# Optimization experiments

Measured on AMD Instinct MI355X. Metric: run time of the kernel, lower is better.

The kernel has to match this reference:

```python
import jax, jax.numpy as jnp
import numpy as np

N_COMPANY = 16384
N_SECTOR = 64
PER_SECTOR = N_COMPANY // N_SECTOR  # 256, companies grouped contiguously by sector
WIN = 32
D_IN = 16
H_GRU = 64
H_INTRA = 64
H_INTER = 64
D_OUT = 4
E_INNER = 524288  # avg degree 32 within sectors


def setup_inputs() -> dict:
    key = jax.random.key(0)
    ks = jax.random.split(key, 20)
    s = 0.05

    daily_data_batch = jax.random.normal(ks[0], (WIN, N_COMPANY, D_IN), jnp.float32)

    rng = np.random.default_rng(0)
    dst = rng.integers(0, N_COMPANY, E_INNER)
    src = (dst // PER_SECTOR) * PER_SECTOR + rng.integers(0, PER_SECTOR, E_INNER)  # same-sector neighbors
    inner_edge = jnp.asarray(np.stack([src, dst]), jnp.int32)

    a, b = np.meshgrid(np.arange(N_SECTOR), np.arange(N_SECTOR), indexing="ij")
    oe = np.stack([a.ravel(), b.ravel()])
    oe = oe[:, oe[0] != oe[1]]  # fully-connected sector graph w/o self loops (GAT adds them)
    outer_edge = jnp.asarray(oe, jnp.int32)

    sector_ids = jnp.asarray(np.arange(N_COMPANY) // PER_SECTOR, jnp.int32)

    inp = {
        "daily_data_batch": daily_data_batch,
        "inner_edge": inner_edge,
        "outer_edge": outer_edge,
        "sector_ids": sector_ids,
        # BatchNorm1d(input_dim*window_size)
        "bn_gamma": jnp.ones((D_IN * WIN,), jnp.float32),
        "bn_beta": jnp.zeros((D_IN * WIN,), jnp.float32),
        # Graph GRU (per-node learnable initial hidden state)
        "gru_Wih": s * jax.random.normal(ks[1], (D_IN, 3 * H_GRU), jnp.float32),
        "gru_Whh": s * jax.random.normal(ks[2], (H_GRU, 3 * H_GRU), jnp.float32),
        "gru_bih": jnp.zeros((3 * H_GRU,), jnp.float32),
        "gru_bhh": jnp.zeros((3 * H_GRU,), jnp.float32),
        "gru_h0": s * jax.random.normal(ks[3], (N_COMPANY, H_GRU), jnp.float32),
        # intra-sector GATConv
        "gat1_W": s * jax.random.normal(ks[4], (H_GRU, H_INTRA), jnp.float32),
        "gat1_asrc": s * jax.random.normal(ks[5], (H_INTRA,), jnp.float32),
        "gat1_adst": s * jax.random.normal(ks[6], (H_INTRA,), jnp.float32),
        "gat1_b": jnp.zeros((H_INTRA,), jnp.float32),
        # inter-sector GATConv
        "gat2_W": s * jax.random.normal(ks[7], (H_INTRA, H_INTER), jnp.float32),
        "gat2_asrc": s * jax.random.normal(ks[8], (H_INTER,), jnp.float32),
        "gat2_adst": s * jax.random.normal(ks[9], (H_INTER,), jnp.float32),
        "gat2_b": jnp.zeros((H_INTER,), jnp.float32),
        # fusion / logit heads
        "fusion_W": s * jax.random.normal(ks[10], (H_GRU + H_INTRA + H_INTER, H_GRU), jnp.float32),
        "fusion_b": jnp.zeros((H_GRU,), jnp.float32),
        "logit_W": s * jax.random.normal(ks[11], (H_GRU, D_OUT), jnp.float32),
        "logit_b": jnp.zeros((D_OUT,), jnp.float32),
    }
    return inp


def _gat(x, edge, W, a_src, a_dst, b):
    """PyG-style single-head GATConv with default add_self_loops=True."""
    N = x.shape[0]
    h = x @ W  # [N, F]
    loops = jnp.arange(N, dtype=edge.dtype)
    src = jnp.concatenate([edge[0], loops])
    dst = jnp.concatenate([edge[1], loops])
    e = jax.nn.leaky_relu(h[src] @ a_src + h[dst] @ a_dst, 0.2)  # [E]
    # segment softmax over incoming edges per dst node
    m = jax.ops.segment_max(e, dst, num_segments=N)
    ex = jnp.exp(e - m[dst])
    denom = jax.ops.segment_sum(ex, dst, num_segments=N)
    alpha = ex / (denom[dst] + 1e-16)
    out = jax.ops.segment_sum(h[src] * alpha[:, None], dst, num_segments=N)
    return out + b


def _forward(daily_data_batch, inner_edge, outer_edge, sector_ids,
             bn_gamma, bn_beta,
             gru_Wih, gru_Whh, gru_bih, gru_bhh, gru_h0,
             gat1_W, gat1_asrc, gat1_adst, gat1_b,
             gat2_W, gat2_asrc, gat2_adst, gat2_b,
             fusion_W, fusion_b, logit_W, logit_b):
    W, N, D = daily_data_batch.shape
    # BatchNorm1d over companies (train-mode batch stats, eps=1e-5)
    xb = jnp.transpose(daily_data_batch, (1, 0, 2)).reshape(N, W * D)
    mu = xb.mean(axis=0)
    var = xb.var(axis=0)
    xb = (xb - mu) * jax.lax.rsqrt(var + 1e-5) * bn_gamma + bn_beta
    x = jnp.transpose(xb.reshape(N, W, D), (1, 0, 2))  # [W, N, D]

    # GRU over the window, per-node hidden state
    def step(h, xt):
        gi = xt @ gru_Wih + gru_bih
        gh = h @ gru_Whh + gru_bhh
        ir, iz, inn = jnp.split(gi, 3, axis=-1)
        hr, hz, hn = jnp.split(gh, 3, axis=-1)
        r = jax.nn.sigmoid(ir + hr)
        z = jax.nn.sigmoid(iz + hz)
        n = jnp.tanh(inn + r * hn)
        return (1.0 - z) * n + z * h, None

    seq_emb, _ = jax.lax.scan(step, gru_h0, x)  # [N, H_GRU]

    intra_emb = _gat(seq_emb, inner_edge, gat1_W, gat1_asrc, gat1_adst, gat1_b)  # [N, H_INTRA]

    # sector_separater + per-sector max pooling == segment_max
    sec_pool = jax.ops.segment_max(intra_emb, sector_ids, num_segments=N_SECTOR)  # [S, H_INTRA]
    sec_emb = _gat(sec_pool, outer_edge, gat2_W, gat2_asrc, gat2_adst, gat2_b)  # [S, H_INTER]
    sec_broad = sec_emb[sector_ids]  # repeat_interleave back to companies

    fusion_vec = jnp.concatenate([seq_emb, sec_broad, intra_emb], axis=-1)
    fusion_vec = jax.nn.relu(fusion_vec @ fusion_W + fusion_b)
    logits = jax.nn.softmax(fusion_vec @ logit_W + logit_b, axis=1)
    logits = jnp.cumsum(logits, axis=1)
    eps = 5e-08
    return jnp.clip(logits, eps, 1.0 - eps)


def reference(daily_data_batch, inner_edge, outer_edge, sector_ids,
              bn_gamma, bn_beta,
              gru_Wih, gru_Whh, gru_bih, gru_bhh, gru_h0,
              gat1_W, gat1_asrc, gat1_adst, gat1_b,
              gat2_W, gat2_asrc, gat2_adst, gat2_b,
              fusion_W, fusion_b, logit_W, logit_b):
    return _forward(daily_data_batch, inner_edge, outer_edge, sector_ids,
                    bn_gamma, bn_beta,
                    gru_Wih, gru_Whh, gru_bih, gru_bhh, gru_h0,
                    gat1_W, gat1_asrc, gat1_adst, gat1_b,
                    gat2_W, gat2_asrc, gat2_adst, gat2_b,
                    fusion_W, fusion_b, logit_W, logit_b)
```

## Files before the change

kernel.cpp:

```cpp
#include <hip/hip_runtime.h>

#define NC 16384
#define WIN 32
#define DI 16
#define EI 524288

typedef unsigned short u16;
typedef unsigned char u8;
typedef unsigned int u32;
typedef __attribute__((ext_vector_type(8))) short bfrag8;
typedef __attribute__((ext_vector_type(4))) float facc4;

__device__ __forceinline__ float bf2f(u16 u) { return __uint_as_float(((u32)u) << 16); }
__device__ __forceinline__ u16 f2bf(float f) {
    u32 u = __float_as_uint(f);
    u += 0x7FFFu + ((u >> 16) & 1u);
    return (u16)(u >> 16);
}
__device__ __forceinline__ float frcp(float x) { return __builtin_amdgcn_rcpf(x); }
__device__ __forceinline__ float lrelu(float x) { return x >= 0.0f ? x : 0.2f * x; }
__device__ __forceinline__ float loadf(const void* p, size_t i, bool f32) {
    return f32 ? ((const float*)p)[i] : bf2f(((const u16*)p)[i]);
}
__device__ __forceinline__ bool is_f32(const void* gamma) {
    return ((const u32*)gamma)[0] == 0x3F800000u;
}

#define O_SCALE 0
#define O_SHIFT 512
#define O_WIH   1024
#define O_WHH   4096
#define O_BIH   16384
#define O_BHH   16576
#define O_G1W   16768
#define O_G1AS  20864
#define O_G1AD  20928
#define O_G1B   20992
#define O_G2W   21056
#define O_G2AS  25152
#define O_G2AD  25216
#define O_G2B   25280
#define O_FB    25344
#define O_LW    25408
#define O_LB    25664
#define O_FW16  25668
#define O_BNACC 31812
#define O_SEQ   40960
#define O_H1    1089536
#define O_INTRA 1613824
#define O_SPOOL 2138112
#define O_AS    2158592
#define O_AD    2174976
#define O_M     2191360

__global__ __launch_bounds__(256) void k_convert(const void* __restrict__ gamma,
                                                 const void* __restrict__ wih,
                                                 const void* __restrict__ whh,
                                                 const void* __restrict__ bih,
                                                 const void* __restrict__ bhh,
                                                 const void* __restrict__ g1w,
                                                 const void* __restrict__ g1as,
                                                 const void* __restrict__ g1ad,
                                                 const void* __restrict__ g1b,
                                                 const void* __restrict__ g2w,
                                                 const void* __restrict__ g2as,
                                                 const void* __restrict__ g2ad,
                                                 const void* __restrict__ g2b,
                                                 const void* __restrict__ fw,
                                                 const void* __restrict__ fb,
                                                 const void* __restrict__ lw,
                                                 const void* __restrict__ lb,
                                                 float* __restrict__ ws) {
    int gt = blockIdx.x * 256 + threadIdx.x;
    const int GS = 64 * 256;
    bool f32 = is_f32(gamma);
    u16* fw16 = (u16*)(ws + O_FW16);
    for (int i = gt; i < 3072; i += GS) ws[O_WIH + i] = loadf(wih, i, f32);
    for (int i = gt; i < 12288; i += GS) {
        ws[O_WHH + i] = loadf(whh, i, f32);
        fw16[i] = f32 ? f2bf(((const float*)fw)[i]) : ((const u16*)fw)[i];
    }
    for (int i = gt; i < 192; i += GS) {
        ws[O_BIH + i] = loadf(bih, i, f32);
        ws[O_BHH + i] = loadf(bhh, i, f32);
    }
    for (int i = gt; i < 4096; i += GS) {
        ws[O_G1W + i] = loadf(g1w, i, f32);
        ws[O_G2W + i] = loadf(g2w, i, f32);
    }
    if (gt < 64) {
        ws[O_G1AS + gt] = loadf(g1as, gt, f32);
        ws[O_G1AD + gt] = loadf(g1ad, gt, f32);
        ws[O_G1B + gt] = loadf(g1b, gt, f32);
        ws[O_G2AS + gt] = loadf(g2as, gt, f32);
        ws[O_G2AD + gt] = loadf(g2ad, gt, f32);
        ws[O_G2B + gt] = loadf(g2b, gt, f32);
        ws[O_FB + gt] = loadf(fb, gt, f32);
    }
    if (gt < 256) ws[O_LW + gt] = loadf(lw, gt, f32);
    if (gt < 4) ws[O_LB + gt] = loadf(lb, gt, f32);
    for (int i = gt; i < 1024; i += GS) ws[O_BNACC + i] = 0.f;
}

__global__ __launch_bounds__(256) void k_bnpart(const void* __restrict__ daily,
                                                const void* __restrict__ gamma,
                                                float* __restrict__ bnacc) {
    __shared__ float rS[256 * 17];
    __shared__ float rQ[256 * 17];
    int w = blockIdx.x >> 2, ch = blockIdx.x & 3;
    int tid = threadIdx.x;
    bool f32 = is_f32(gamma);
    float s[16], q[16];
#pragma unroll
    for (int i = 0; i < 16; i++) { s[i] = 0.f; q[i] = 0.f; }
    for (int it = 0; it < 16; it++) {
        int c = ch * 4096 + it * 256 + tid;
        size_t base = ((size_t)w * NC + c) * DI;
        float v[16];
        if (f32) {
            const float4* p = (const float4*)((const float*)daily + base);
            float4 a = p[0], b = p[1], cc = p[2], d = p[3];
            v[0] = a.x; v[1] = a.y; v[2] = a.z; v[3] = a.w;
            v[4] = b.x; v[5] = b.y; v[6] = b.z; v[7] = b.w;
            v[8] = cc.x; v[9] = cc.y; v[10] = cc.z; v[11] = cc.w;
            v[12] = d.x; v[13] = d.y; v[14] = d.z; v[15] = d.w;
        } else {
            const uint4* p = (const uint4*)((const u16*)daily + base);
            uint4 a = p[0], b = p[1];
            u32 us[8] = {a.x, a.y, a.z, a.w, b.x, b.y, b.z, b.w};
#pragma unroll
            for (int i = 0; i < 8; i++) {
                v[2 * i] = __uint_as_float(us[i] << 16);
                v[2 * i + 1] = __uint_as_float(us[i] & 0xFFFF0000u);
            }
        }
#pragma unroll
        for (int i = 0; i < 16; i++) { s[i] += v[i]; q[i] += v[i] * v[i]; }
    }
#pragma unroll
    for (int i = 0; i < 16; i++) { rS[tid * 17 + i] = s[i]; rQ[tid * 17 + i] = q[i]; }
    __syncthreads();
    int f = tid & 15, g = tid >> 4;
    float ss = 0.f, qq = 0.f;
    for (int t = g * 16; t < g * 16 + 16; t++) { ss += rS[t * 17 + f]; qq += rQ[t * 17 + f]; }
    atomicAdd(&bnacc[w * 16 + f], ss);
    atomicAdd(&bnacc[512 + w * 16 + f], qq);
}

__global__ __launch_bounds__(256) void k_edge(const int* __restrict__ edges, u32* __restrict__ M32) {
    int g = blockIdx.x * 256 + threadIdx.x;
    int4 s4 = ((const int4*)edges)[g];
    int4 d4 = ((const int4*)(edges + EI))[g];
    int ss[4] = {s4.x, s4.y, s4.z, s4.w};
    int dd[4] = {d4.x, d4.y, d4.z, d4.w};
#pragma unroll
    for (int i = 0; i < 4; i++) {
        int sl = ss[i] & 255;
        atomicAdd(&M32[dd[i] * 64 + (sl >> 2)], 1u << ((sl & 3) * 8));
    }
}

__global__ __launch_bounds__(256, 4) void k_gru(const void* __restrict__ daily,
                                                const void* __restrict__ gamma,
                                                const void* __restrict__ beta,
                                                const void* __restrict__ h0_g,
                                                const float* __restrict__ ws,
                                                float* __restrict__ seq_out,
                                                u16* __restrict__ h1_out,
                                                float* __restrict__ asg,
                                                float* __restrict__ adg) {
    __shared__ __attribute__((aligned(16))) u16 sHd[2][16 * 72];
    __shared__ __attribute__((aligned(16))) u16 sXall[512 * 24];
    __shared__ float sSc[512], sSh[512];
    __shared__ float sRed[2][4][16];
    int tid = threadIdx.x;
    int w = tid >> 6, lane = tid & 63;
    int li = lane & 15, q = lane >> 4;
    int col = w * 16 + li;
    int n0 = blockIdx.x * 16;
    bool f32 = is_f32(gamma);

    for (int f = tid; f < 512; f += 256) {
        float mu = ws[O_BNACC + f] * (1.0f / NC);
        float var = ws[O_BNACC + 512 + f] * (1.0f / NC) - mu * mu;
        float sc = loadf(gamma, f, f32) * rsqrtf(var + 1e-5f);
        sSc[f] = sc;
        sSh[f] = loadf(beta, f, f32) - mu * sc;
    }
    __syncthreads();
    for (int R = tid; R < 512; R += 256) {
        int t = R >> 4, m = R & 15;
        size_t base = ((size_t)t * NC + n0 + m) * DI;
        float xv[16];
        if (f32) {
            const float4* p = (const float4*)((const float*)daily + base);
            float4 a = p[0], b = p[1], c = p[2], d = p[3];
            xv[0] = a.x; xv[1] = a.y; xv[2] = a.z; xv[3] = a.w;
            xv[4] = b.x; xv[5] = b.y; xv[6] = b.z; xv[7] = b.w;
            xv[8] = c.x; xv[9] = c.y; xv[10] = c.z; xv[11] = c.w;
            xv[12] = d.x; xv[13] = d.y; xv[14] = d.z; xv[15] = d.w;
        } else {
            const uint4* p = (const uint4*)((const u16*)daily + base);
            uint4 a = p[0], b = p[1];
            u32 us[8] = {a.x, a.y, a.z, a.w, b.x, b.y, b.z, b.w};
#pragma unroll
            for (int i = 0; i < 8; i++) {
                xv[2 * i] = __uint_as_float(us[i] << 16);
                xv[2 * i + 1] = __uint_as_float(us[i] & 0xFFFF0000u);
            }
        }
        u16 px[16];
#pragma unroll
        for (int i = 0; i < 16; i++) px[i] = f2bf(xv[i] * sSc[t * 16 + i] + sSh[t * 16 + i]);
        *(uint4*)&sXall[R * 24] = *(const uint4*)&px[0];
        *(uint4*)&sXall[R * 24 + 8] = *(const uint4*)&px[8];
    }

    bfrag8 bh[3][2], bx[3];
#pragma unroll
    for (int g = 0; g < 3; g++) {
        float sc = (g < 2) ? -1.0f : -2.0f;
#pragma unroll
        for (int kc = 0; kc < 2; kc++)
#pragma unroll
            for (int j = 0; j < 8; j++) {
                int k = kc * 32 + q * 8 + j;
                bh[g][kc][j] = (short)f2bf(sc * ws[O_WHH + k * 192 + g * 64 + col]);
            }
#pragma unroll
        for (int j = 0; j < 8; j++) {
            int k = q * 8 + j;
            bx[g][j] = (k < 16) ? (short)f2bf(sc * ws[O_WIH + k * 192 + g * 64 + col]) : (short)0;
        }
    }
    float bR = -1.0f * (ws[O_BIH + col] + ws[O_BHH + col]);
    float bZ = -1.0f * (ws[O_BIH + 64 + col] + ws[O_BHH + 64 + col]);
    float bNX = -2.0f * ws[O_BIH + 128 + col];
    float bNH = -2.0f * ws[O_BHH + 128 + col];

    float hC[4];
#pragma unroll
    for (int r = 0; r < 4; r++)
        hC[r] = loadf(h0_g, (size_t)(n0 + q * 4 + r) * 64 + col, f32);
    if (tid < 128) {
        int hr = tid >> 3, hc = (tid & 7) * 8;
        u16 hrow[8];
#pragma unroll
        for (int i = 0; i < 8; i++)
            hrow[i] = f2bf(loadf(h0_g, (size_t)(n0 + hr) * 64 + hc + i, f32));
        *(uint4*)&sHd[0][hr * 72 + hc] = *(const uint4*)&hrow[0];
    }
    __syncthreads();

    bool xl = (q < 2);
    for (int t = 0; t < WIN; t++) {
        int p = t & 1;
        bfrag8 ax = (bfrag8){0, 0, 0, 0, 0, 0, 0, 0};
        if (xl) ax = *(const bfrag8*)&sXall[(t * 16 + li) * 24 + q * 8];
        bfrag8 ah0 = *(const bfrag8*)&sHd[p][li * 72 + q * 8];
        bfrag8 ah1 = *(const bfrag8*)&sHd[p][li * 72 + 32 + q * 8];
        facc4 aR = __builtin_amdgcn_mfma_f32_16x16x32_bf16(ah0, bh[0][0], (facc4){bR, bR, bR, bR}, 0, 0, 0);
        facc4 aZ = __builtin_amdgcn_mfma_f32_16x16x32_bf16(ah0, bh[1][0], (facc4){bZ, bZ, bZ, bZ}, 0, 0, 0);
        facc4 aNH = __builtin_amdgcn_mfma_f32_16x16x32_bf16(ah0, bh[2][0], (facc4){bNH, bNH, bNH, bNH}, 0, 0, 0);
        facc4 aNX = __builtin_amdgcn_mfma_f32_16x16x32_bf16(ax, bx[2], (facc4){bNX, bNX, bNX, bNX}, 0, 0, 0);
        aR = __builtin_amdgcn_mfma_f32_16x16x32_bf16(ah1, bh[0][1], aR, 0, 0, 0);
        aZ = __builtin_amdgcn_mfma_f32_16x16x32_bf16(ah1, bh[1][1], aZ, 0, 0, 0);
        aNH = __builtin_amdgcn_mfma_f32_16x16x32_bf16(ah1, bh[2][1], aNH, 0, 0, 0);
        aR = __builtin_amdgcn_mfma_f32_16x16x32_bf16(ax, bx[0], aR, 0, 0, 0);
        aZ = __builtin_amdgcn_mfma_f32_16x16x32_bf16(ax, bx[1], aZ, 0, 0, 0);
#pragma unroll
        for (int r = 0; r < 4; r++) {
            float gr = frcp(1.0f + __expf(aR[r]));
            float gz = frcp(1.0f + __expf(aZ[r]));
            float narg = aNX[r] + gr * aNH[r];
            float gn = 2.0f * frcp(1.0f + __expf(narg)) - 1.0f;
            hC[r] = gn + gz * (hC[r] - gn);
        }
#pragma unroll
        for (int r = 0; r < 4; r++)
            sHd[p ^ 1][(q * 4 + r) * 72 + col] = f2bf(hC[r]);
        __syncthreads();
    }

#pragma unroll
    for (int r = 0; r < 4; r++)
        seq_out[(size_t)(n0 + q * 4 + r) * 64 + col] = hC[r];

    const facc4 zf = {0.f, 0.f, 0.f, 0.f};
    bfrag8 a0 = *(const bfrag8*)&sHd[0][li * 72 + q * 8];
    bfrag8 a1 = *(const bfrag8*)&sHd[0][li * 72 + 32 + q * 8];
    bfrag8 bg0, bg1;
#pragma unroll
    for (int j = 0; j < 8; j++) {
        bg0[j] = (short)f2bf(ws[O_G1W + (q * 8 + j) * 64 + col]);
        bg1[j] = (short)f2bf(ws[O_G1W + (32 + q * 8 + j) * 64 + col]);
    }
    facc4 acc = __builtin_amdgcn_mfma_f32_16x16x32_bf16(a0, bg0, zf, 0, 0, 0);
    acc = __builtin_amdgcn_mfma_f32_16x16x32_bf16(a1, bg1, acc, 0, 0, 0);
    float a1s_j = ws[O_G1AS + col], a1d_j = ws[O_G1AD + col];
    float pAs[4], pAd[4];
#pragma unroll
    for (int r = 0; r < 4; r++) {
        h1_out[(size_t)(n0 + q * 4 + r) * 64 + col] = f2bf(acc[r]);
        pAs[r] = acc[r] * a1s_j;
        pAd[r] = acc[r] * a1d_j;
    }
#pragma unroll
    for (int o = 1; o < 16; o <<= 1) {
#pragma unroll
        for (int r = 0; r < 4; r++) {
            pAs[r] += __shfl_xor(pAs[r], o);
            pAd[r] += __shfl_xor(pAd[r], o);
        }
    }
    if (li == 0) {
#pragma unroll
        for (int r = 0; r < 4; r++) {
            sRed[0][w][q * 4 + r] = pAs[r];
            sRed[1][w][q * 4 + r] = pAd[r];
        }
    }
    __syncthreads();
    if (tid < 16) {
        asg[n0 + tid] = sRed[0][0][tid] + sRed[0][1][tid] + sRed[0][2][tid] + sRed[0][3][tid];
        adg[n0 + tid] = sRed[1][0][tid] + sRed[1][1][tid] + sRed[1][2][tid] + sRed[1][3][tid];
    }
}

__global__ __launch_bounds__(256) void k_gat1agg(const u16* __restrict__ h1g,
                                                 const float* __restrict__ ws,
                                                 const u8* __restrict__ M8,
                                                 const float* __restrict__ asg,
                                                 const float* __restrict__ adg,
                                                 u16* __restrict__ intra,
                                                 float* __restrict__ spool4) {
    __shared__ __attribute__((aligned(16))) u16 hT[64 * 264];
    __shared__ __attribute__((aligned(16))) u16 sP[64 * 136];
    __shared__ float sAs[256], sAd[64], sB[64], sRS[64];
    __shared__ float sRSp[4][64];
    __shared__ float wmax[4];
    int tid = threadIdx.x;
    int sector = blockIdx.x >> 2;
    int dstbase = sector * 256 + (blockIdx.x & 3) * 64;
    int sbase = sector * 256;
    {
        const u16* row = h1g + (size_t)(sbase + tid) * 64;
#pragma unroll
        for (int c = 0; c < 16; c++) {
            uint2 v = ((const uint2*)row)[c];
            hT[(c * 4 + 0) * 264 + tid] = (u16)(v.x & 0xffff);
            hT[(c * 4 + 1) * 264 + tid] = (u16)(v.x >> 16);
            hT[(c * 4 + 2) * 264 + tid] = (u16)(v.y & 0xffff);
            hT[(c * 4 + 3) * 264 + tid] = (u16)(v.y >> 16);
        }
    }
    sAs[tid] = asg[sbase + tid];
    if (tid < 64) { sAd[tid] = adg[dstbase + tid]; sB[tid] = ws[O_G1B + tid]; }
    __syncthreads();
    int lane = tid & 63, w = tid >> 6;
    int li = lane & 15, q = lane >> 4;
    {
        float a = sAs[tid];
#pragma unroll
        for (int o = 1; o < 64; o <<= 1) a = fmaxf(a, __shfl_xor(a, o));
        if (lane == 0) wmax[w] = a;
    }
    __syncthreads();
    float maxA = fmaxf(fmaxf(wmax[0], wmax[1]), fmaxf(wmax[2], wmax[3]));

    int prow = tid >> 2, pcg = tid & 3;
    float adr_p = sAd[prow];
    float mrow_p = lrelu(maxA + adr_p);
    float lsum = 0.f;

    facc4 acc[4];
#pragma unroll
    for (int mt = 0; mt < 4; mt++) acc[mt] = (facc4){0.f, 0.f, 0.f, 0.f};

#pragma unroll
    for (int half = 0; half < 2; half++) {
        const u8* mp = M8 + (size_t)(dstbase + prow) * 256 + half * 128 + pcg * 32;
        uint4 mva = *(const uint4*)mp;
        uint4 mvb = *(const uint4*)(mp + 16);
        u32 wsrc[8] = {mva.x, mva.y, mva.z, mva.w, mvb.x, mvb.y, mvb.z, mvb.w};
#pragma unroll
        for (int i2 = 0; i2 < 16; i2++) {
            int i0 = 2 * i2;
            u32 mb0 = (wsrc[i0 >> 2] >> ((i0 & 3) * 8)) & 255u;
            u32 mb1 = (wsrc[i0 >> 2] >> (((i0 + 1) & 3) * 8)) & 255u;
            int c = half * 128 + pcg * 32 + i0;
            float e0 = lrelu(sAs[c] + adr_p);
            float e1 = lrelu(sAs[c + 1] + adr_p);
            float v0 = (float)mb0 * __expf(e0 - mrow_p);
            float v1 = (float)mb1 * __expf(e1 - mrow_p);
            u16 b0 = f2bf(v0), b1 = f2bf(v1);
            *(u32*)&sP[prow * 136 + pcg * 32 + i0] = (u32)b0 | ((u32)b1 << 16);
            lsum += bf2f(b0) + bf2f(b1);
        }
        __syncthreads();
#pragma unroll
        for (int kc = 0; kc < 4; kc++) {
            bfrag8 bfh = *(const bfrag8*)&hT[(w * 16 + li) * 264 + half * 128 + kc * 32 + q * 8];
#pragma unroll
            for (int mt = 0; mt < 4; mt++) {
                bfrag8 af = *(const bfrag8*)&sP[(mt * 16 + li) * 136 + kc * 32 + q * 8];
                acc[mt] = __builtin_amdgcn_mfma_f32_16x16x32_bf16(af, bfh, acc[mt], 0, 0, 0);
            }
        }
        __syncthreads();
    }
    sRSp[pcg][prow] = lsum;
    __syncthreads();
    if (tid < 64) sRS[tid] = sRSp[0][tid] + sRSp[1][tid] + sRSp[2][tid] + sRSp[3][tid];
    __syncthreads();

    float vmax = -1e30f;
    int colL = w * 16 + li;
#pragma unroll
    for (int mt = 0; mt < 4; mt++) {
#pragma unroll
        for (int r = 0; r < 4; r++) {
            int row = mt * 16 + q * 4 + r;
            int d = dstbase + row;
            int selfI = (blockIdx.x & 3) * 64 + row;
            float adr = sAd[row];
            float es = lrelu(sAs[selfI] + adr);
            float mrow = lrelu(maxA + adr);
            float exS = __expf(es - mrow);
            float denom = sRS[row] + exS;
            float inv = frcp(denom + 1e-16f);
            float selfh = bf2f(hT[colL * 264 + selfI]);
            float val = (acc[mt][r] + exS * selfh) * inv + sB[colL];
            intra[(size_t)d * 64 + colL] = f2bf(val);
            vmax = fmaxf(vmax, val);
        }
    }
    vmax = fmaxf(vmax, __shfl_xor(vmax, 16));
    vmax = fmaxf(vmax, __shfl_xor(vmax, 32));
    if (q == 0) spool4[(size_t)blockIdx.x * 64 + colL] = vmax;
}

__global__ __launch_bounds__(256) void k_fusion(const float* __restrict__ seq,
                                                const float* __restrict__ spool4,
                                                const u16* __restrict__ intra,
                                                const float* __restrict__ ws,
                                                const void* __restrict__ gamma,
                                                void* __restrict__ out) {
    __shared__ __attribute__((aligned(16))) union {
        struct { float sPt[4096]; float sW2[4096]; float sH2[4096]; } p0;
        struct { u16 sV[64 * 200]; float sFus[64 * 68]; } p1;
    } U;
    __shared__ float sSemb[64], sAs2[64], sAd2[64];
    __shared__ float sFB[64], sLW[256], sLB[4];
    __shared__ float red2[512];
    int tid = threadIdx.x, n0 = blockIdx.x * 64;
    int sid = blockIdx.x >> 2;
    bool f32 = is_f32(gamma);

    for (int i = tid; i < 4096; i += 256) {
        int n = i >> 6, k = i & 63;
        float m = fmaxf(fmaxf(spool4[(n * 4 + 0) * 64 + k], spool4[(n * 4 + 1) * 64 + k]),
                        fmaxf(spool4[(n * 4 + 2) * 64 + k], spool4[(n * 4 + 3) * 64 + k]));
        U.p0.sPt[k * 64 + n] = m;
        U.p0.sW2[i] = ws[O_G2W + i];
    }
    __syncthreads();
    {
        int n = tid >> 2, jg = tid & 3, j0 = jg * 16;
        float acc0[16];
#pragma unroll
        for (int i = 0; i < 16; i++) acc0[i] = 0.f;
        for (int k = 0; k < 64; k++) {
            float a = U.p0.sPt[k * 64 + n];
#pragma unroll
            for (int i = 0; i < 16; i += 4) {
                float4 w4 = *(const float4*)&U.p0.sW2[k * 64 + j0 + i];
                acc0[i] += a * w4.x; acc0[i + 1] += a * w4.y; acc0[i + 2] += a * w4.z; acc0[i + 3] += a * w4.w;
            }
        }
#pragma unroll
        for (int i = 0; i < 16; i++) U.p0.sH2[n * 64 + j0 + i] = acc0[i];
        float ps = 0.f, pd = 0.f;
#pragma unroll
        for (int i = 0; i < 16; i++) { ps += acc0[i] * ws[O_G2AS + j0 + i]; pd += acc0[i] * ws[O_G2AD + j0 + i]; }
        red2[(n * 4 + jg) * 2] = ps;
        red2[(n * 4 + jg) * 2 + 1] = pd;
    }
    __syncthreads();
    if (tid < 64) {
        float s = 0.f, dd = 0.f;
        for (int g = 0; g < 4; g++) { s += red2[(tid * 4 + g) * 2]; dd += red2[(tid * 4 + g) * 2 + 1]; }
        sAs2[tid] = s; sAd2[tid] = dd;
    }
    __syncthreads();
    if (tid < 64) {
        float e = lrelu(sAs2[tid] + sAd2[sid]);
        float m = e;
        for (int o = 32; o; o >>= 1) m = fmaxf(m, __shfl_xor(m, o));
        float ex = __expf(e - m);
        float den = ex;
        for (int o = 32; o; o >>= 1) den += __shfl_xor(den, o);
        float inv = frcp(den + 1e-16f);
        float o_ = 0.f;
        for (int l = 0; l < 64; l++) {
            float a = __shfl(ex, l);
            o_ += a * U.p0.sH2[l * 64 + tid];
        }
        sSemb[tid] = o_ * inv + ws[O_G2B + tid];
    }
    if (tid < 64) sFB[tid] = ws[O_FB + tid];
    sLW[tid] = ws[O_LW + tid];
    if (tid < 4) sLB[tid] = ws[O_LB + tid];
    __syncthreads();

    {
        int c = tid >> 2, p = tid & 3;
        u16 px[16];
        const float* rp = seq + (size_t)(n0 + c) * 64 + p * 16;
#pragma unroll
        for (int i = 0; i < 16; i += 4) {
            float4 v = *(const float4*)&rp[i];
            px[i] = f2bf(v.x); px[i + 1] = f2bf(v.y); px[i + 2] = f2bf(v.z); px[i + 3] = f2bf(v.w);
        }
        *(uint4*)&U.p1.sV[c * 200 + p * 16] = *(const uint4*)&px[0];
        *(uint4*)&U.p1.sV[c * 200 + p * 16 + 8] = *(const uint4*)&px[8];
#pragma unroll
        for (int i = 0; i < 16; i++) px[i] = f2bf(sSemb[p * 16 + i]);
        *(uint4*)&U.p1.sV[c * 200 + 64 + p * 16] = *(const uint4*)&px[0];
        *(uint4*)&U.p1.sV[c * 200 + 64 + p * 16 + 8] = *(const uint4*)&px[8];
        const u16* ip = intra + (size_t)(n0 + c) * 64 + p * 16;
        *(uint4*)&U.p1.sV[c * 200 + 128 + p * 16] = *(const uint4*)ip;
        *(uint4*)&U.p1.sV[c * 200 + 128 + p * 16 + 8] = *(const uint4*)(ip + 8);
    }
    int lane = tid & 63, w = tid >> 6;
    int li = lane & 15, q = lane >> 4;
    int colw = w * 16 + li;
    const u16* fw16g = (const u16*)(ws + O_FW16);
    bfrag8 bwf[6];
#pragma unroll
    for (int kc = 0; kc < 6; kc++)
#pragma unroll
        for (int j = 0; j < 8; j++)
            bwf[kc][j] = (short)fw16g[(kc * 32 + q * 8 + j) * 64 + colw];
    __syncthreads();

    facc4 acc[4];
#pragma unroll
    for (int mt = 0; mt < 4; mt++) acc[mt] = (facc4){0.f, 0.f, 0.f, 0.f};
#pragma unroll
    for (int kc = 0; kc < 6; kc++) {
#pragma unroll
        for (int mt = 0; mt < 4; mt++) {
            bfrag8 av = *(const bfrag8*)&U.p1.sV[(mt * 16 + li) * 200 + kc * 32 + q * 8];
            acc[mt] = __builtin_amdgcn_mfma_f32_16x16x32_bf16(av, bwf[kc], acc[mt], 0, 0, 0);
        }
    }
    float fb = sFB[colw];
#pragma unroll
    for (int mt = 0; mt < 4; mt++)
#pragma unroll
        for (int r = 0; r < 4; r++) {
            float v = fmaxf(acc[mt][r] + fb, 0.f);
            U.p1.sFus[(mt * 16 + q * 4 + r) * 68 + colw] = v;
        }
    __syncthreads();

    if (tid < 64) {
        float l[4] = {sLB[0], sLB[1], sLB[2], sLB[3]};
        for (int j = 0; j < 64; j++) {
            float v = U.p1.sFus[tid * 68 + j];
            l[0] += v * sLW[j * 4 + 0];
            l[1] += v * sLW[j * 4 + 1];
            l[2] += v * sLW[j * 4 + 2];
            l[3] += v * sLW[j * 4 + 3];
        }
        float m = fmaxf(fmaxf(l[0], l[1]), fmaxf(l[2], l[3]));
        float e0 = __expf(l[0] - m), e1 = __expf(l[1] - m), e2 = __expf(l[2] - m), e3 = __expf(l[3] - m);
        float is = frcp(e0 + e1 + e2 + e3);
        float c0 = e0 * is;
        float c1 = c0 + e1 * is;
        float c2 = c1 + e2 * is;
        float c3 = c2 + e3 * is;
        const float lo = 5e-8f, hi = 1.0f - 5e-8f;
        c0 = fminf(fmaxf(c0, lo), hi);
        c1 = fminf(fmaxf(c1, lo), hi);
        c2 = fminf(fmaxf(c2, lo), hi);
        c3 = fminf(fmaxf(c3, lo), hi);
        size_t ob = (size_t)(n0 + tid) * 4;
        if (f32) {
            *(float4*)&((float*)out)[ob] = make_float4(c0, c1, c2, c3);
        } else {
            *(ushort4*)&((u16*)out)[ob] = make_ushort4(f2bf(c0), f2bf(c1), f2bf(c2), f2bf(c3));
        }
    }
}

extern "C" void kernel_launch(void* const* d_in, const int* in_sizes, int n_in,
                              void* d_out, int out_size, void* d_ws, size_t ws_size,
                              hipStream_t stream) {
    const void* daily = d_in[0];
    const int* inner = (const int*)d_in[1];
    const void* gamma = d_in[4];
    const void* beta = d_in[5];
    const void* wih = d_in[6];
    const void* whh = d_in[7];
    const void* bih = d_in[8];
    const void* bhh = d_in[9];
    const void* h0 = d_in[10];
    const void* g1w = d_in[11];
    const void* g1as = d_in[12];
    const void* g1ad = d_in[13];
    const void* g1b = d_in[14];
    const void* g2w = d_in[15];
    const void* g2as = d_in[16];
    const void* g2ad = d_in[17];
    const void* g2b = d_in[18];
    const void* fw = d_in[19];
    const void* fb = d_in[20];
    const void* lw = d_in[21];
    const void* lb = d_in[22];

    float* ws = (float*)d_ws;
    u16* h1g = (u16*)(ws + O_H1);
    u16* intra = (u16*)(ws + O_INTRA);
    u8* M8 = (u8*)(ws + O_M);

    hipMemsetAsync((void*)M8, 0, (size_t)NC * 256, stream);
    k_convert<<<64, 256, 0, stream>>>(gamma, wih, whh, bih, bhh, g1w, g1as, g1ad, g1b,
                                      g2w, g2as, g2ad, g2b, fw, fb, lw, lb, ws);
    k_bnpart<<<128, 256, 0, stream>>>(daily, gamma, ws + O_BNACC);
    k_edge<<<512, 256, 0, stream>>>(inner, (u32*)M8);
    k_gru<<<1024, 256, 0, stream>>>(daily, gamma, beta, h0, ws, ws + O_SEQ, h1g, ws + O_AS, ws + O_AD);
    k_gat1agg<<<256, 256, 0, stream>>>(h1g, ws, M8, ws + O_AS, ws + O_AD, intra, ws + O_SPOOL);
    k_fusion<<<256, 256, 0, stream>>>(ws + O_SEQ, ws + O_SPOOL, intra, ws, gamma, d_out);
}
```

Before: 228.9 us.

## Merge prep kernels, split GAT aggregation finer, use MFMA for sector GAT projection

Drops the separate memset by zeroing the adjacency byte matrix inside the convert kernel, and merges the BN partial-sum and edge-count kernels into one launch. The intra-sector GAT aggregation now uses 512 blocks of 32 destination rows, covering all 256 sources in one pass with a single sync instead of two 128-source halves. The fusion kernel computes the sector-pool projection with bf16 MFMA instead of scalar FMA loops, which lowers its precision. Together these cut launch count and per-block serial work and raise parallelism, but each GAT block now restages the full sector's h1 tile for half as many rows.

```diff
diff --git a/kernel.cpp b/kernel.cpp
--- a/kernel.cpp
+++ b/kernel.cpp
@@ -49,9 +49,9 @@
 #define O_H1    1089536
 #define O_INTRA 1613824
 #define O_SPOOL 2138112
-#define O_AS    2158592
-#define O_AD    2174976
-#define O_M     2191360
+#define O_AS    2170880
+#define O_AD    2187264
+#define O_M     2203648
 
 __global__ __launch_bounds__(256) void k_convert(const void* __restrict__ gamma,
                                                  const void* __restrict__ wih,
@@ -70,7 +70,8 @@
                                                  const void* __restrict__ fb,
                                                  const void* __restrict__ lw,
                                                  const void* __restrict__ lb,
-                                                 float* __restrict__ ws) {
+                                                 float* __restrict__ ws,
+                                                 uint4* __restrict__ M16) {
     int gt = blockIdx.x * 256 + threadIdx.x;
     const int GS = 64 * 256;
     bool f32 = is_f32(gamma);
@@ -100,15 +101,33 @@
     if (gt < 256) ws[O_LW + gt] = loadf(lw, gt, f32);
     if (gt < 4) ws[O_LB + gt] = loadf(lb, gt, f32);
     for (int i = gt; i < 1024; i += GS) ws[O_BNACC + i] = 0.f;
-}
-
-__global__ __launch_bounds__(256) void k_bnpart(const void* __restrict__ daily,
-                                                const void* __restrict__ gamma,
-                                                float* __restrict__ bnacc) {
+    const uint4 z4 = {0u, 0u, 0u, 0u};
+    for (int i = gt; i < 262144; i += GS) M16[i] = z4;
+}
+
+__global__ __launch_bounds__(256) void k_prep(const void* __restrict__ daily,
+                                              const void* __restrict__ gamma,
+                                              float* __restrict__ bnacc,
+                                              const int* __restrict__ edges,
+                                              u32* __restrict__ M32) {
     __shared__ float rS[256 * 17];
     __shared__ float rQ[256 * 17];
-    int w = blockIdx.x >> 2, ch = blockIdx.x & 3;
+    int bid = blockIdx.x;
     int tid = threadIdx.x;
+    if (bid >= 128) {
+        int g = (bid - 128) * 256 + tid;
+        int4 s4 = ((const int4*)edges)[g];
+        int4 d4 = ((const int4*)(edges + EI))[g];
+        int ss[4] = {s4.x, s4.y, s4.z, s4.w};
+        int dd[4] = {d4.x, d4.y, d4.z, d4.w};
+#pragma unroll
+        for (int i = 0; i < 4; i++) {
+            int sl = ss[i] & 255;
+            atomicAdd(&M32[dd[i] * 64 + (sl >> 2)], 1u << ((sl & 3) * 8));
+        }
+        return;
+    }
+    int w = bid >> 2, ch = bid & 3;
     bool f32 = is_f32(gamma);
     float s[16], q[16];
 #pragma unroll
@@ -145,19 +164,6 @@
     for (int t = g * 16; t < g * 16 + 16; t++) { ss += rS[t * 17 + f]; qq += rQ[t * 17 + f]; }
     atomicAdd(&bnacc[w * 16 + f], ss);
     atomicAdd(&bnacc[512 + w * 16 + f], qq);
-}
-
-__global__ __launch_bounds__(256) void k_edge(const int* __restrict__ edges, u32* __restrict__ M32) {
-    int g = blockIdx.x * 256 + threadIdx.x;
-    int4 s4 = ((const int4*)edges)[g];
-    int4 d4 = ((const int4*)(edges + EI))[g];
-    int ss[4] = {s4.x, s4.y, s4.z, s4.w};
-    int dd[4] = {d4.x, d4.y, d4.z, d4.w};
-#pragma unroll
-    for (int i = 0; i < 4; i++) {
-        int sl = ss[i] & 255;
-        atomicAdd(&M32[dd[i] * 64 + (sl >> 2)], 1u << ((sl & 3) * 8));
-    }
 }
 
 __global__ __launch_bounds__(256, 4) void k_gru(const void* __restrict__ daily,
@@ -333,15 +339,15 @@
                                                  const float* __restrict__ asg,
                                                  const float* __restrict__ adg,
                                                  u16* __restrict__ intra,
-                                                 float* __restrict__ spool4) {
+                                                 float* __restrict__ spool8) {
     __shared__ __attribute__((aligned(16))) u16 hT[64 * 264];
-    __shared__ __attribute__((aligned(16))) u16 sP[64 * 136];
-    __shared__ float sAs[256], sAd[64], sB[64], sRS[64];
-    __shared__ float sRSp[4][64];
+    __shared__ __attribute__((aligned(16))) u16 sP[32 * 264];
+    __shared__ float sAs[256], sAd[32], sB[64], sRS[32];
+    __shared__ float sRSp[8][32];
     __shared__ float wmax[4];
     int tid = threadIdx.x;
-    int sector = blockIdx.x >> 2;
-    int dstbase = sector * 256 + (blockIdx.x & 3) * 64;
+    int sector = blockIdx.x >> 3;
+    int dstbase = sector * 256 + (blockIdx.x & 7) * 32;
     int sbase = sector * 256;
     {
         const u16* row = h1g + (size_t)(sbase + tid) * 64;
@@ -355,7 +361,8 @@
         }
     }
     sAs[tid] = asg[sbase + tid];
-    if (tid < 64) { sAd[tid] = adg[dstbase + tid]; sB[tid] = ws[O_G1B + tid]; }
+    if (tid < 32) sAd[tid] = adg[dstbase + tid];
+    if (tid < 64) sB[tid] = ws[O_G1B + tid];
     __syncthreads();
     int lane = tid & 63, w = tid >> 6;
     int li = lane & 15, q = lane >> 4;
@@ -368,18 +375,12 @@
     __syncthreads();
     float maxA = fmaxf(fmaxf(wmax[0], wmax[1]), fmaxf(wmax[2], wmax[3]));
 
-    int prow = tid >> 2, pcg = tid & 3;
-    float adr_p = sAd[prow];
-    float mrow_p = lrelu(maxA + adr_p);
-    float lsum = 0.f;
-
-    facc4 acc[4];
-#pragma unroll
-    for (int mt = 0; mt < 4; mt++) acc[mt] = (facc4){0.f, 0.f, 0.f, 0.f};
-
-#pragma unroll
-    for (int half = 0; half < 2; half++) {
-        const u8* mp = M8 + (size_t)(dstbase + prow) * 256 + half * 128 + pcg * 32;
+    int prow = tid >> 3, pcg = tid & 7;
+    {
+        float adr_p = sAd[prow];
+        float mrow_p = lrelu(maxA + adr_p);
+        float lsum = 0.f;
+        const u8* mp = M8 + (size_t)(dstbase + prow) * 256 + pcg * 32;
         uint4 mva = *(const uint4*)mp;
         uint4 mvb = *(const uint4*)(mp + 16);
         u32 wsrc[8] = {mva.x, mva.y, mva.z, mva.w, mvb.x, mvb.y, mvb.z, mvb.w};
@@ -388,41 +389,48 @@
             int i0 = 2 * i2;
             u32 mb0 = (wsrc[i0 >> 2] >> ((i0 & 3) * 8)) & 255u;
             u32 mb1 = (wsrc[i0 >> 2] >> (((i0 + 1) & 3) * 8)) & 255u;
-            int c = half * 128 + pcg * 32 + i0;
+            int c = pcg * 32 + i0;
             float e0 = lrelu(sAs[c] + adr_p);
             float e1 = lrelu(sAs[c + 1] + adr_p);
             float v0 = (float)mb0 * __expf(e0 - mrow_p);
             float v1 = (float)mb1 * __expf(e1 - mrow_p);
             u16 b0 = f2bf(v0), b1 = f2bf(v1);
-            *(u32*)&sP[prow * 136 + pcg * 32 + i0] = (u32)b0 | ((u32)b1 << 16);
+            *(u32*)&sP[prow * 264 + pcg * 32 + i0] = (u32)b0 | ((u32)b1 << 16);
             lsum += bf2f(b0) + bf2f(b1);
         }
-        __syncthreads();
-#pragma unroll
-        for (int kc = 0; kc < 4; kc++) {
-            bfrag8 bfh = *(const bfrag8*)&hT[(w * 16 + li) * 264 + half * 128 + kc * 32 + q * 8];
-#pragma unroll
-            for (int mt = 0; mt < 4; mt++) {
-                bfrag8 af = *(const bfrag8*)&sP[(mt * 16 + li) * 136 + kc * 32 + q * 8];
-                acc[mt] = __builtin_amdgcn_mfma_f32_16x16x32_bf16(af, bfh, acc[mt], 0, 0, 0);
-            }
-        }
-        __syncthreads();
-    }
-    sRSp[pcg][prow] = lsum;
-    __syncthreads();
-    if (tid < 64) sRS[tid] = sRSp[0][tid] + sRSp[1][tid] + sRSp[2][tid] + sRSp[3][tid];
+        sRSp[pcg][prow] = lsum;
+    }
+    __syncthreads();
+
+    facc4 acc[2];
+    acc[0] = (facc4){0.f, 0.f, 0.f, 0.f};
+    acc[1] = (facc4){0.f, 0.f, 0.f, 0.f};
+#pragma unroll
+    for (int kc = 0; kc < 8; kc++) {
+        bfrag8 bfh = *(const bfrag8*)&hT[(w * 16 + li) * 264 + kc * 32 + q * 8];
+#pragma unroll
+        for (int mt = 0; mt < 2; mt++) {
+            bfrag8 af = *(const bfrag8*)&sP[(mt * 16 + li) * 264 + kc * 32 + q * 8];
+            acc[mt] = __builtin_amdgcn_mfma_f32_16x16x32_bf16(af, bfh, acc[mt], 0, 0, 0);
+        }
+    }
+    if (tid < 32) {
+        float s = 0.f;
+#pragma unroll
+        for (int g = 0; g < 8; g++) s += sRSp[g][tid];
+        sRS[tid] = s;
+    }
     __syncthreads();
 
     float vmax = -1e30f;
     int colL = w * 16 + li;
 #pragma unroll
-    for (int mt = 0; mt < 4; mt++) {
+    for (int mt = 0; mt < 2; mt++) {
 #pragma unroll
         for (int r = 0; r < 4; r++) {
             int row = mt * 16 + q * 4 + r;
             int d = dstbase + row;
-            int selfI = (blockIdx.x & 3) * 64 + row;
+            int selfI = (blockIdx.x & 7) * 32 + row;
             float adr = sAd[row];
             float es = lrelu(sAs[selfI] + adr);
             float mrow = lrelu(maxA + adr);
@@ -437,17 +445,17 @@
     }
     vmax = fmaxf(vmax, __shfl_xor(vmax, 16));
     vmax = fmaxf(vmax, __shfl_xor(vmax, 32));
-    if (q == 0) spool4[(size_t)blockIdx.x * 64 + colL] = vmax;
+    if (q == 0) spool8[(size_t)blockIdx.x * 64 + colL] = vmax;
 }
 
 __global__ __launch_bounds__(256) void k_fusion(const float* __restrict__ seq,
-                                                const float* __restrict__ spool4,
+                                                const float* __restrict__ spool8,
                                                 const u16* __restrict__ intra,
                                                 const float* __restrict__ ws,
                                                 const void* __restrict__ gamma,
                                                 void* __restrict__ out) {
     __shared__ __attribute__((aligned(16))) union {
-        struct { float sPt[4096]; float sW2[4096]; float sH2[4096]; } p0;
+        struct { u16 sPmax[64 * 72]; float sH2[64 * 68]; } p0;
         struct { u16 sV[64 * 200]; float sFus[64 * 68]; } p1;
     } U;
     __shared__ float sSemb[64], sAs2[64], sAd2[64];
@@ -456,33 +464,48 @@
     int tid = threadIdx.x, n0 = blockIdx.x * 64;
     int sid = blockIdx.x >> 2;
     bool f32 = is_f32(gamma);
+    int lane = tid & 63, w = tid >> 6;
+    int li = lane & 15, q = lane >> 4;
+    int colw = w * 16 + li;
 
     for (int i = tid; i < 4096; i += 256) {
         int n = i >> 6, k = i & 63;
-        float m = fmaxf(fmaxf(spool4[(n * 4 + 0) * 64 + k], spool4[(n * 4 + 1) * 64 + k]),
-                        fmaxf(spool4[(n * 4 + 2) * 64 + k], spool4[(n * 4 + 3) * 64 + k]));
-        U.p0.sPt[k * 64 + n] = m;
-        U.p0.sW2[i] = ws[O_G2W + i];
+        const float* pp = &spool8[(size_t)(n * 8) * 64 + k];
+        float m = pp[0];
+#pragma unroll
+        for (int p = 1; p < 8; p++) m = fmaxf(m, pp[p * 64]);
+        U.p0.sPmax[n * 72 + k] = f2bf(m);
+    }
+    bfrag8 bw2[2];
+#pragma unroll
+    for (int kc = 0; kc < 2; kc++)
+#pragma unroll
+        for (int j = 0; j < 8; j++)
+            bw2[kc][j] = (short)f2bf(ws[O_G2W + (kc * 32 + q * 8 + j) * 64 + colw]);
+    __syncthreads();
+    {
+        const facc4 zf = {0.f, 0.f, 0.f, 0.f};
+#pragma unroll
+        for (int mt = 0; mt < 4; mt++) {
+            bfrag8 af0 = *(const bfrag8*)&U.p0.sPmax[(mt * 16 + li) * 72 + q * 8];
+            bfrag8 af1 = *(const bfrag8*)&U.p0.sPmax[(mt * 16 + li) * 72 + 32 + q * 8];
+            facc4 a2 = __builtin_amdgcn_mfma_f32_16x16x32_bf16(af0, bw2[0], zf, 0, 0, 0);
+            a2 = __builtin_amdgcn_mfma_f32_16x16x32_bf16(af1, bw2[1], a2, 0, 0, 0);
+#pragma unroll
+            for (int r = 0; r < 4; r++)
+                U.p0.sH2[(mt * 16 + q * 4 + r) * 68 + colw] = a2[r];
+        }
     }
     __syncthreads();
     {
         int n = tid >> 2, jg = tid & 3, j0 = jg * 16;
-        float acc0[16];
-#pragma unroll
-        for (int i = 0; i < 16; i++) acc0[i] = 0.f;
-        for (int k = 0; k < 64; k++) {
-            float a = U.p0.sPt[k * 64 + n];
-#pragma unroll
-            for (int i = 0; i < 16; i += 4) {
-                float4 w4 = *(const float4*)&U.p0.sW2[k * 64 + j0 + i];
-                acc0[i] += a * w4.x; acc0[i + 1] += a * w4.y; acc0[i + 2] += a * w4.z; acc0[i + 3] += a * w4.w;
-            }
-        }
-#pragma unroll
-        for (int i = 0; i < 16; i++) U.p0.sH2[n * 64 + j0 + i] = acc0[i];
         float ps = 0.f, pd = 0.f;
 #pragma unroll
-        for (int i = 0; i < 16; i++) { ps += acc0[i] * ws[O_G2AS + j0 + i]; pd += acc0[i] * ws[O_G2AD + j0 + i]; }
+        for (int i = 0; i < 16; i++) {
+            float v = U.p0.sH2[n * 68 + j0 + i];
+            ps += v * ws[O_G2AS + j0 + i];
+            pd += v * ws[O_G2AD + j0 + i];
+        }
         red2[(n * 4 + jg) * 2] = ps;
         red2[(n * 4 + jg) * 2 + 1] = pd;
     }
@@ -504,7 +527,7 @@
         float o_ = 0.f;
         for (int l = 0; l < 64; l++) {
             float a = __shfl(ex, l);
-            o_ += a * U.p0.sH2[l * 64 + tid];
+            o_ += a * U.p0.sH2[l * 68 + tid];
         }
         sSemb[tid] = o_ * inv + ws[O_G2B + tid];
     }
@@ -532,9 +555,6 @@
         *(uint4*)&U.p1.sV[c * 200 + 128 + p * 16] = *(const uint4*)ip;
         *(uint4*)&U.p1.sV[c * 200 + 128 + p * 16 + 8] = *(const uint4*)(ip + 8);
     }
-    int lane = tid & 63, w = tid >> 6;
-    int li = lane & 15, q = lane >> 4;
-    int colw = w * 16 + li;
     const u16* fw16g = (const u16*)(ws + O_FW16);
     bfrag8 bwf[6];
 #pragma unroll
@@ -625,12 +645,10 @@
     u16* intra = (u16*)(ws + O_INTRA);
     u8* M8 = (u8*)(ws + O_M);
 
-    hipMemsetAsync((void*)M8, 0, (size_t)NC * 256, stream);
     k_convert<<<64, 256, 0, stream>>>(gamma, wih, whh, bih, bhh, g1w, g1as, g1ad, g1b,
-                                      g2w, g2as, g2ad, g2b, fw, fb, lw, lb, ws);
-    k_bnpart<<<128, 256, 0, stream>>>(daily, gamma, ws + O_BNACC);
-    k_edge<<<512, 256, 0, stream>>>(inner, (u32*)M8);
+                                      g2w, g2as, g2ad, g2b, fw, fb, lw, lb, ws, (uint4*)M8);
+    k_prep<<<640, 256, 0, stream>>>(daily, gamma, ws + O_BNACC, inner, (u32*)M8);
     k_gru<<<1024, 256, 0, stream>>>(daily, gamma, beta, h0, ws, ws + O_SEQ, h1g, ws + O_AS, ws + O_AD);
-    k_gat1agg<<<256, 256, 0, stream>>>(h1g, ws, M8, ws + O_AS, ws + O_AD, intra, ws + O_SPOOL);
+    k_gat1agg<<<512, 256, 0, stream>>>(h1g, ws, M8, ws + O_AS, ws + O_AD, intra, ws + O_SPOOL);
     k_fusion<<<256, 256, 0, stream>>>(ws + O_SEQ, ws + O_SPOOL, intra, ws, gamma, d_out);
 }
```

After: 218.7 us. -4.5%, faster.
